# Kernel tuning notes

Hardware: AMD Instinct MI355X
Metric: run time of the kernel (lower is better)

## Reference

```python
import jax, jax.numpy as jnp
import numpy as np

EPS = 1e-5
NUM_GRAPHS = 64


def _linear(x, W, b):
    return x @ W + b


def setup_inputs() -> dict:
    key = jax.random.key(0)
    ks = jax.random.split(key, 32)
    N, E, IN, EF, H, ED, T, L, C = 25000, 400000, 128, 16, 32, 32, 4, 2, 1
    F = H            # F_in (divide_input=False)
    Fo = H // T      # F_out per tower

    def w(k, shape):
        return jax.random.normal(k, shape, jnp.float32) / np.sqrt(shape[-2])

    inp = {
        'x': jax.random.normal(ks[0], (N, IN), jnp.float32),
        'edge_attr': jax.random.normal(ks[1], (E, EF), jnp.float32),
        'edge_weight': jax.random.uniform(ks[2], (E,), jnp.float32),
        'edge_index': jax.random.randint(ks[3], (2, E), 0, N),
        'batch': jnp.sort(jax.random.randint(ks[4], (N,), 0, NUM_GRAPHS)),
        'node_W': w(ks[5], (IN, H)), 'node_b': jnp.zeros((H,), jnp.float32),
        'edge_W': w(ks[6], (EF, ED)), 'edge_b': jnp.zeros((ED,), jnp.float32),
        'enc_W': w(ks[7], (L, ED, F)), 'enc_b': jnp.zeros((L, F), jnp.float32),
        'pre_W': w(ks[8], (L, T, 3 * F, F)), 'pre_b': jnp.zeros((L, T, F), jnp.float32),
        'post_W': w(ks[9], (L, T, 13 * F, Fo)), 'post_b': jnp.zeros((L, T, Fo), jnp.float32),
        'lin_W': w(ks[10], (L, H, H)), 'lin_b': jnp.zeros((L, H), jnp.float32),
        'bn_g': jnp.ones((L, H), jnp.float32), 'bn_b': jnp.zeros((L, H), jnp.float32),
        'mlp_W1': w(ks[11], (H, H)), 'mlp_b1': jnp.zeros((H,), jnp.float32),
        'mlp_W2': w(ks[12], (H, H // 2)), 'mlp_b2': jnp.zeros((H // 2,), jnp.float32),
        'mlp_W3': w(ks[13], (H // 2, C)), 'mlp_b3': jnp.zeros((C,), jnp.float32),
    }
    return inp


def reference(x, edge_attr, edge_weight, node_W, node_b, edge_W, edge_b,
              enc_W, enc_b, pre_W, pre_b, post_W, post_b, lin_W, lin_b,
              bn_g, bn_b, mlp_W1, mlp_b1, mlp_W2, mlp_b2, mlp_W3, mlp_b3,
              edge_index, batch):
    N = x.shape[0]
    L, T = pre_W.shape[0], pre_W.shape[1]
    src, dst = edge_index[0], edge_index[1]

    # degree-based scalers (PNA): avg_deg_log = mean_n log(deg_n + 1)
    deg = jax.ops.segment_sum(jnp.ones((src.shape[0],), x.dtype), dst, num_segments=N)
    avg_deg_log = jnp.mean(jnp.log(deg + 1.0))
    degc = jnp.clip(deg, 1.0)[:, None, None]          # [N,1,1]
    log_deg = jnp.log(degc + 1.0)
    amp = log_deg / avg_deg_log                        # amplification scaler
    att = avg_deg_log / log_deg                        # attenuation scaler
    has_edge = (deg > 0)[:, None, None]

    h = _linear(x, node_W, node_b)                     # node_emb  [N,H]
    e = _linear(edge_attr, edge_W, edge_b)             # edge_emb  [E,ED]

    for l in range(L):
        el = _linear(e, enc_W[l], enc_b[l])            # edge_encoder [E,F]
        m_in = jnp.concatenate([h[dst], h[src], el], axis=-1)      # [E,3F]
        msg = jnp.einsum('ef,tfg->etg', m_in, pre_W[l]) + pre_b[l]  # per-tower pre_nn [E,T,F]
        msg = msg * edge_weight[:, None, None]
        s = jax.ops.segment_sum(msg, dst, num_segments=N)
        s2 = jax.ops.segment_sum(msg * msg, dst, num_segments=N)
        mean = s / degc
        std = jnp.sqrt(jax.nn.relu(s2 / degc - mean * mean) + EPS)
        mn = jnp.where(has_edge, jax.ops.segment_min(msg, dst, num_segments=N), 0.0)
        mx = jnp.where(has_edge, jax.ops.segment_max(msg, dst, num_segments=N), 0.0)
        agg = jnp.concatenate([mean, mn, mx, std], axis=-1)            # [N,T,4F]
        agg = jnp.concatenate([agg, agg * amp, agg * att], axis=-1)    # [N,T,12F]
        out = jnp.concatenate(
            [jnp.broadcast_to(h[:, None, :], (N, T, h.shape[-1])), agg], axis=-1)  # [N,T,13F]
        out = jnp.einsum('ntf,tfg->ntg', out, post_W[l]) + post_b[l]   # post_nn [N,T,Fo]
        out = out.reshape(N, -1) @ lin_W[l] + lin_b[l]                 # [N,H]
        mu = jnp.mean(out, axis=0)
        var = jnp.var(out, axis=0)
        out = (out - mu) / jnp.sqrt(var + EPS) * bn_g[l] + bn_b[l]     # BatchNorm (batch stats)
        h = jax.nn.relu(out)

    g = jax.ops.segment_sum(h, batch, num_segments=NUM_GRAPHS)        # global_add_pool
    g = jax.nn.relu(_linear(g, mlp_W1, mlp_b1))
    g = jax.nn.relu(_linear(g, mlp_W2, mlp_b2))
    return _linear(g, mlp_W3, mlp_b3)
```

## Files before the change

kernel.cpp:

```cpp
#include <hip/hip_runtime.h>

constexpr float kEps = 1e-5f;

typedef float f2v __attribute__((ext_vector_type(2)));

__device__ __forceinline__ unsigned short f2bf(float x) {
  unsigned int u = __float_as_uint(x);
  unsigned int r = (u + 0x7fffu + ((u >> 16) & 1u)) >> 16;
  return (unsigned short)r;
}
__device__ __forceinline__ float bflo(unsigned int u) { return __uint_as_float(u << 16); }
__device__ __forceinline__ float bfhi(unsigned int u) { return __uint_as_float(u & 0xffff0000u); }
__device__ __forceinline__ unsigned int packbf(float a, float b) {
  return (unsigned int)f2bf(a) | ((unsigned int)f2bf(b) << 16);
}
__device__ __forceinline__ f2v fma2(f2v a, f2v b, f2v c) { return __builtin_elementwise_fma(a, b, c); }
__device__ __forceinline__ f2v splat2(float x) { f2v r; r.x = x; r.y = x; return r; }
__device__ __forceinline__ f2v unpk(unsigned int u) { f2v r; r.x = bflo(u); r.y = bfhi(u); return r; }
__device__ __forceinline__ f2v min2(f2v a, f2v b) { return __builtin_elementwise_min(a, b); }
__device__ __forceinline__ f2v max2(f2v a, f2v b) { return __builtin_elementwise_max(a, b); }


__global__ void zero_kernel(int* __restrict__ a, int* __restrict__ b,
                            float* __restrict__ bnb, int n) {
  int i = blockIdx.x * blockDim.x + threadIdx.x;
  if (i < n) { a[i] = 0; b[i] = 0; }
  if (i < 128) bnb[i] = 0.f;
}

__global__ void hist_kernel(const int* __restrict__ dst, int* __restrict__ deg, int E) {
  int e = blockIdx.x * blockDim.x + threadIdx.x;
  if (e < E) atomicAdd(&deg[dst[e]], 1);
}

__global__ void scan1_kernel(const int* __restrict__ deg, int* __restrict__ off,
                             int* __restrict__ part, int N) {
  __shared__ int sm[1024];
  int i = blockIdx.x * 1024 + threadIdx.x;
  int v = (i < N) ? deg[i] : 0;
  sm[threadIdx.x] = v;
  __syncthreads();
  for (int o = 1; o < 1024; o <<= 1) {
    int t = (threadIdx.x >= o) ? sm[threadIdx.x - o] : 0;
    __syncthreads();
    sm[threadIdx.x] += t;
    __syncthreads();
  }
  if (i < N) off[i] = sm[threadIdx.x] - v;
  if (threadIdx.x == 1023) part[blockIdx.x] = sm[1023];
}

__global__ void scan2_kernel(int* __restrict__ part, int* __restrict__ off, int nb, int N) {
  if (threadIdx.x == 0) {
    int run = 0;
    for (int b = 0; b < nb; b++) { int p = part[b]; part[b] = run; run += p; }
    off[N] = run;
  }
}

__global__ void scan3_kernel(int* __restrict__ off, const int* __restrict__ part, int N) {
  int i = blockIdx.x * 1024 + threadIdx.x;
  if (i < N) off[i] += part[blockIdx.x];
}

__global__ void fill_kernel(const int* __restrict__ src, const int* __restrict__ dst,
                            const float* __restrict__ ew, const float4* __restrict__ eattr4,
                            const int* __restrict__ off, int* __restrict__ cnt,
                            int* __restrict__ srcs, float* __restrict__ ews,
                            float4* __restrict__ eattrg4, int E) {
  int e = blockIdx.x * blockDim.x + threadIdx.x;
  if (e < E) {
    int d = dst[e];
    int slot = off[d] + atomicAdd(&cnt[d], 1);
    srcs[slot] = src[e];
    ews[slot] = ew[e];
    float4 a = eattr4[e * 4 + 0], b = eattr4[e * 4 + 1];
    float4 c = eattr4[e * 4 + 2], q = eattr4[e * 4 + 3];
    eattrg4[(size_t)slot * 4 + 0] = a;
    eattrg4[(size_t)slot * 4 + 1] = b;
    eattrg4[(size_t)slot * 4 + 2] = c;
    eattrg4[(size_t)slot * 4 + 3] = q;
  }
}

__global__ void adl_kernel(const int* __restrict__ deg, float* __restrict__ adl, int N) {
  __shared__ float sm[1024];
  float s = 0.f;
  for (int n = threadIdx.x; n < N; n += 1024) s += logf((float)deg[n] + 1.f);
  sm[threadIdx.x] = s;
  __syncthreads();
  for (int o = 512; o > 0; o >>= 1) {
    if (threadIdx.x < o) sm[threadIdx.x] += sm[threadIdx.x + o];
    __syncthreads();
  }
  if (threadIdx.x == 0) adl[0] = sm[0];
}

__global__ void node_emb_kernel(const float* __restrict__ x, const float* __restrict__ W,
                                const float* __restrict__ b, float* __restrict__ h, int N) {
  int n = blockIdx.x * 8 + (threadIdx.x >> 5);
  int j = threadIdx.x & 31;
  if (n >= N) return;
  float acc = b[j];
  const float4* x4 = (const float4*)(x + (size_t)n * 128);
#pragma unroll
  for (int q = 0; q < 32; q++) {
    float4 v = x4[q];
    acc += v.x * W[(4 * q + 0) * 32 + j];
    acc += v.y * W[(4 * q + 1) * 32 + j];
    acc += v.z * W[(4 * q + 2) * 32 + j];
    acc += v.w * W[(4 * q + 3) * 32 + j];
  }
  h[n * 32 + j] = acc;
}

__global__ void fuse_kernel(const float* __restrict__ edge_W, const float* __restrict__ edge_b,
                            const float* __restrict__ enc_W, const float* __restrict__ enc_b,
                            const float* __restrict__ pre_W, const float* __restrict__ pre_b,
                            float* __restrict__ Wf, float* __restrict__ bf) {
  __shared__ float tW[2][16][32];
  __shared__ float tb[2][32];
  int tid = threadIdx.x;
  for (int i = tid; i < 1024; i += 256) {
    int l = i >> 9, r = (i >> 5) & 15, c = i & 31;
    float s = 0.f;
    for (int k = 0; k < 32; k++) s += edge_W[r * 32 + k] * enc_W[(l * 32 + k) * 32 + c];
    tW[l][r][c] = s;
  }
  for (int i = tid; i < 64; i += 256) {
    int l = i >> 5, c = i & 31;
    float s = enc_b[l * 32 + c];
    for (int k = 0; k < 32; k++) s += edge_b[k] * enc_W[(l * 32 + k) * 32 + c];
    tb[l][c] = s;
  }
  __syncthreads();
  for (int i = tid; i < 4096; i += 256) {
    int l = i >> 11, t = (i >> 9) & 3, r = (i >> 5) & 15, c = i & 31;
    float s = 0.f;
    for (int k = 0; k < 32; k++) s += tW[l][r][k] * pre_W[((l * 4 + t) * 96 + 64 + k) * 32 + c];
    Wf[i] = s;
  }
  for (int i = tid; i < 256; i += 256) {
    int l = i >> 7, t = (i >> 5) & 3, c = i & 31;
    float s = pre_b[(l * 4 + t) * 32 + c];
    for (int k = 0; k < 32; k++) s += tb[l][k] * pre_W[((l * 4 + t) * 96 + 64 + k) * 32 + c];
    bf[i] = s;
  }
}

__global__ __launch_bounds__(256) void prep_kernel(
    const float* __restrict__ h, const float* __restrict__ preW,
    const float* __restrict__ bfv, unsigned short* __restrict__ qB,
    unsigned short* __restrict__ AB, int N) {
  __shared__ float hs[16][32];
  int tid = threadIdx.x;
  int c = tid & 127, half = tid >> 7;
  int t = c >> 5, g = c & 31;
  float ws[32], wd[32];
  {
    const float* pS = preW + (t * 96 + 32) * 32 + g;
    const float* pD = preW + (t * 96) * 32 + g;
#pragma unroll
    for (int k = 0; k < 32; k++) { ws[k] = pS[k * 32]; wd[k] = pD[k * 32]; }
  }
  float bc = bfv[c];
  int base = blockIdx.x * 16;
  for (int i = tid; i < 512; i += 256) {
    int nn = i >> 5;
    hs[nn][i & 31] = (base + nn < N) ? h[(size_t)(base + nn) * 32 + (i & 31)] : 0.f;
  }
  __syncthreads();
#pragma unroll
  for (int nn = 0; nn < 8; ++nn) {
    int nl = half + 2 * nn;
    int n = base + nl;
    if (n >= N) continue;
    float qa = 0.f, Aa = bc;
#pragma unroll
    for (int k = 0; k < 32; k++) {
      float hk = hs[nl][k];
      qa = fmaf(hk, ws[k], qa);
      Aa = fmaf(hk, wd[k], Aa);
    }
    qB[(size_t)n * 128 + c] = f2bf(qa);
    AB[(size_t)n * 128 + c] = f2bf(Aa);
  }
}

__global__ __launch_bounds__(256) void bnprep_kernel(
    const float* __restrict__ pre, const float* __restrict__ bnv,
    const float* __restrict__ gamma, const float* __restrict__ beta,
    const float* __restrict__ preW, const float* __restrict__ bfv,
    float* __restrict__ h, unsigned short* __restrict__ qB,
    unsigned short* __restrict__ AB, int N) {
  __shared__ float hs[16][32];
  int tid = threadIdx.x;
  int base = blockIdx.x * 16;
  float invN = 1.f / (float)N;
  for (int idx = tid; idx < 512; idx += 256) {
    int nn = idx >> 5, j = idx & 31;
    int n = base + nn;
    float v = 0.f;
    if (n < N) {
      float mu = bnv[j] * invN;
      float var = bnv[32 + j] * invN - mu * mu;
      float is = rsqrtf(var + kEps);
      v = fmaxf((pre[(size_t)n * 32 + j] - mu) * is * gamma[j] + beta[j], 0.f);
      h[(size_t)n * 32 + j] = v;
    }
    hs[nn][j] = v;
  }
  int c = tid & 127, half = tid >> 7;
  int t = c >> 5, g = c & 31;
  float ws[32], wd[32];
  {
    const float* pS = preW + (t * 96 + 32) * 32 + g;
    const float* pD = preW + (t * 96) * 32 + g;
#pragma unroll
    for (int k = 0; k < 32; k++) { ws[k] = pS[k * 32]; wd[k] = pD[k * 32]; }
  }
  float bc = bfv[c];
  __syncthreads();
#pragma unroll
  for (int nn = 0; nn < 8; ++nn) {
    int nl = half + 2 * nn;
    int n = base + nl;
    if (n >= N) continue;
    float qa = 0.f, Aa = bc;
#pragma unroll
    for (int k = 0; k < 32; k++) {
      float hk = hs[nl][k];
      qa = fmaf(hk, ws[k], qa);
      Aa = fmaf(hk, wd[k], Aa);
    }
    qB[(size_t)n * 128 + c] = f2bf(qa);
    AB[(size_t)n * 128 + c] = f2bf(Aa);
  }
}

#define FOLDE(F, EA, EB, EC, ED)                                \
  F = fma2(splat2(EA.x), wf[0], F);  F = fma2(splat2(EA.y), wf[1], F);  \
  F = fma2(splat2(EA.z), wf[2], F);  F = fma2(splat2(EA.w), wf[3], F);  \
  F = fma2(splat2(EB.x), wf[4], F);  F = fma2(splat2(EB.y), wf[5], F);  \
  F = fma2(splat2(EB.z), wf[6], F);  F = fma2(splat2(EB.w), wf[7], F);  \
  F = fma2(splat2(EC.x), wf[8], F);  F = fma2(splat2(EC.y), wf[9], F);  \
  F = fma2(splat2(EC.z), wf[10], F); F = fma2(splat2(EC.w), wf[11], F); \
  F = fma2(splat2(ED.x), wf[12], F); F = fma2(splat2(ED.y), wf[13], F); \
  F = fma2(splat2(ED.z), wf[14], F); F = fma2(splat2(ED.w), wf[15], F);

#define STAT2(V)                                                \
  sum = sum + V; sq = fma2(V, V, sq); mn = min2(mn, V); mx = max2(mx, V);

__global__ __launch_bounds__(256, 3) void agg4_kernel(
    const unsigned int* __restrict__ qB, const unsigned int* __restrict__ AB,
    const int* __restrict__ coff, const int* __restrict__ srcs,
    const float* __restrict__ ews, const float* __restrict__ eattrg,
    const float* __restrict__ Wf, unsigned int* __restrict__ stats, int N) {
  int lane = threadIdx.x & 63;
  int n = (blockIdx.x * blockDim.x + threadIdx.x) >> 6;
  if (n >= N) return;
  int t = lane >> 4, g0 = (2 * lane) & 31;
  f2v wf[16];
  {
    const float* p = Wf + t * 512 + g0;
#pragma unroll
    for (int k = 0; k < 16; k++) { f2v r; r.x = p[k * 32]; r.y = p[k * 32 + 1]; wf[k] = r; }
  }
  f2v a = unpk(AB[(size_t)n * 64 + lane]);
  int beg = coff[n], end = coff[n + 1];
  int dg = end - beg;
  f2v sum = splat2(0.f), sq = splat2(0.f);
  f2v mn = splat2(1e30f), mx = splat2(-1e30f);

  int i = beg;
  int sc0 = 0, sc1 = 0, sc2 = 0, sc3 = 0;
  float w0 = 0.f, w1 = 0.f, w2 = 0.f, w3 = 0.f;
  if (i + 4 <= end) {
    sc0 = srcs[i]; sc1 = srcs[i + 1]; sc2 = srcs[i + 2]; sc3 = srcs[i + 3];
    w0 = ews[i]; w1 = ews[i + 1]; w2 = ews[i + 2]; w3 = ews[i + 3];
  }
  for (; i + 4 <= end; i += 4) {
    unsigned int q0 = qB[(size_t)sc0 * 64 + lane];
    unsigned int q1 = qB[(size_t)sc1 * 64 + lane];
    unsigned int q2 = qB[(size_t)sc2 * 64 + lane];
    unsigned int q3 = qB[(size_t)sc3 * 64 + lane];
    const float4* ep = (const float4*)(eattrg + (size_t)i * 16);
    float4 e0 = ep[0], e1 = ep[1], e2 = ep[2], e3 = ep[3];
    float4 e4 = ep[4], e5 = ep[5], e6 = ep[6], e7 = ep[7];
    float4 e8 = ep[8], e9 = ep[9], e10 = ep[10], e11 = ep[11];
    float4 e12 = ep[12], e13 = ep[13], e14 = ep[14], e15 = ep[15];
    float wc0 = w0, wc1 = w1, wc2 = w2, wc3 = w3;
    if (i + 8 <= end) {
      sc0 = srcs[i + 4]; sc1 = srcs[i + 5]; sc2 = srcs[i + 6]; sc3 = srcs[i + 7];
      w0 = ews[i + 4]; w1 = ews[i + 5]; w2 = ews[i + 6]; w3 = ews[i + 7];
    }
    __builtin_amdgcn_sched_barrier(0);
    f2v f0 = splat2(0.f), f1 = splat2(0.f), f2_ = splat2(0.f), f3 = splat2(0.f);
    FOLDE(f0, e0, e1, e2, e3)
    FOLDE(f1, e4, e5, e6, e7)
    FOLDE(f2_, e8, e9, e10, e11)
    FOLDE(f3, e12, e13, e14, e15)
    f2v v;
    v = (a + unpk(q0) + f0) * splat2(wc0); STAT2(v)
    v = (a + unpk(q1) + f1) * splat2(wc1); STAT2(v)
    v = (a + unpk(q2) + f2_) * splat2(wc2); STAT2(v)
    v = (a + unpk(q3) + f3) * splat2(wc3); STAT2(v)
  }
  for (; i < end; ++i) {
    int s = srcs[i];
    float w = ews[i];
    unsigned int q = qB[(size_t)s * 64 + lane];
    const float4* ep = (const float4*)(eattrg + (size_t)i * 16);
    float4 ea = ep[0], eb = ep[1], ec = ep[2], ed = ep[3];
    f2v f = splat2(0.f);
    FOLDE(f, ea, eb, ec, ed)
    f2v v = (a + unpk(q) + f) * splat2(w);
    STAT2(v)
  }
  if (dg == 0) { mn = splat2(0.f); mx = splat2(0.f); }
  float inv = 1.f / (float)(dg > 0 ? dg : 1);
  f2v mean = sum * splat2(inv);
  f2v var = sq * splat2(inv) - mean * mean;
  float sd0 = sqrtf(fmaxf(var.x, 0.f) + kEps);
  float sd1 = sqrtf(fmaxf(var.y, 0.f) + kEps);
  unsigned int* sp = stats + (size_t)n * 256;
  sp[0 * 64 + lane] = packbf(mean.x, mean.y);
  sp[1 * 64 + lane] = packbf(mn.x, mn.y);
  sp[2 * 64 + lane] = packbf(mx.x, mx.y);
  sp[3 * 64 + lane] = packbf(sd0, sd1);
}

__global__ __launch_bounds__(256) void post_kernel(
    const float* __restrict__ h, const unsigned int* __restrict__ stats,
    const int* __restrict__ coff, const float* __restrict__ adl,
    const float* __restrict__ postW, const float* __restrict__ postB,
    const float* __restrict__ linW, const float* __restrict__ linB,
    float* __restrict__ pre, float* __restrict__ bn, int N) {
  __shared__ unsigned int pwp[208 * 32];
  __shared__ unsigned int stu[4][256];
  __shared__ float red[8][32];
  int tid = threadIdx.x;
  for (int i = tid; i < 6656; i += 256) {
    int r = i >> 5, cc = i & 31, tP = cc >> 3, gq = cc & 7;
    float lo = postW[tP * 3328 + (2 * r) * 8 + gq];
    float hi = postW[tP * 3328 + (2 * r + 1) * 8 + gq];
    pwp[i] = packbf(lo, hi);
  }
  __syncthreads();

  int wave = tid >> 6, lane = tid & 63;
  int c = lane & 31, hh = lane >> 5;
  int tP = c >> 3;
  float adN = adl[0];
  float bs = 0.f, bq = 0.f;

  for (int n = blockIdx.x * 4 + wave; n < N; n += gridDim.x * 4) {
    {
      uint4 su = ((const uint4*)stats)[(size_t)n * 64 + lane];
      ((uint4*)stu[wave])[lane] = su;
    }
    int dg = coff[n + 1] - coff[n];
    float degc = (float)(dg > 0 ? dg : 1);
    float ad = adN / (float)N;
    float ld = logf(degc + 1.f);
    float amp = ld / ad, att = ad / ld;

    float acc = (hh == 0) ? postB[tP * 8 + (c & 7)] : 0.f;
    const float4* h4 = (const float4*)(h + (size_t)n * 32);
#pragma unroll
    for (int q4 = 0; q4 < 4; q4++) {
      float4 hv = h4[hh * 4 + q4];
      int r0 = hh * 8 + q4 * 2;
      unsigned int u0 = pwp[r0 * 32 + c], u1 = pwp[(r0 + 1) * 32 + c];
      acc = fmaf(hv.x, bflo(u0), acc);
      acc = fmaf(hv.y, bfhi(u0), acc);
      acc = fmaf(hv.z, bflo(u1), acc);
      acc = fmaf(hv.w, bfhi(u1), acc);
    }
#pragma unroll 8
    for (int jj = 0; jj < 32; jj++) {
      int sIdx = hh * 2 + (jj >> 4);
      unsigned int sv = stu[wave][sIdx * 64 + tP * 16 + (jj & 15)];
      float v0 = bflo(sv), v1 = bfhi(sv);
      int rm = 16 + hh * 32 + jj, ra = 80 + hh * 32 + jj, rt = 144 + hh * 32 + jj;
      unsigned int um = pwp[rm * 32 + c];
      unsigned int ua = pwp[ra * 32 + c];
      unsigned int ut = pwp[rt * 32 + c];
      float w0 = bflo(um); w0 = fmaf(amp, bflo(ua), w0); w0 = fmaf(att, bflo(ut), w0);
      float w1 = bfhi(um); w1 = fmaf(amp, bfhi(ua), w1); w1 = fmaf(att, bfhi(ut), w1);
      acc = fmaf(v0, w0, acc);
      acc = fmaf(v1, w1, acc);
    }
    acc += __shfl_xor(acc, 32);
    float o = linB[c];
#pragma unroll
    for (int k = 0; k < 32; k++) {
      float a = __shfl(acc, k);
      o = fmaf(a, linW[k * 32 + c], o);
    }
    if (lane < 32) {
      pre[(size_t)n * 32 + c] = o;
      bs += o;
      bq = fmaf(o, o, bq);
    }
  }

  __syncthreads();
  if (lane < 32) {
    red[wave * 2 + 0][c] = bs;
    red[wave * 2 + 1][c] = bq;
  }
  __syncthreads();
  if (tid < 64) {
    int which = tid >> 5, cc = tid & 31;
    float s = red[0 * 2 + which][cc] + red[1 * 2 + which][cc] +
              red[2 * 2 + which][cc] + red[3 * 2 + which][cc];
    atomicAdd(&bn[which * 32 + cc], s);
  }
}

__global__ void bn_apply_kernel(const float* __restrict__ pre, const float* __restrict__ bn,
                                const float* __restrict__ gamma, const float* __restrict__ beta,
                                float* __restrict__ h, int N) {
  int i = blockIdx.x * 256 + threadIdx.x;
  if (i >= N * 32) return;
  int j = i & 31;
  float invN = 1.f / (float)N;
  float mu = bn[j] * invN;
  float var = bn[32 + j] * invN - mu * mu;
  float is = rsqrtf(var + kEps);
  float v = (pre[i] - mu) * is * gamma[j] + beta[j];
  h[i] = fmaxf(v, 0.f);
}


__device__ __forceinline__ int lower_bound_dev(const int* a, int n, int key) {
  int lo = 0, hi = n;
  while (lo < hi) {
    int m = (lo + hi) >> 1;
    if (a[m] < key) lo = m + 1; else hi = m;
  }
  return lo;
}

__global__ void pool_kernel(const float* __restrict__ h, const int* __restrict__ batch,
                            float* __restrict__ gp, int N) {
  int gi = blockIdx.x;
  int lo = lower_bound_dev(batch, N, gi);
  int hi = lower_bound_dev(batch, N, gi + 1);
  __shared__ float part[8][32];
  int j = threadIdx.x & 31, ch = threadIdx.x >> 5;
  float s = 0.f;
  for (int n = lo + ch; n < hi; n += 8) s += h[(size_t)n * 32 + j];
  part[ch][j] = s;
  __syncthreads();
  if (threadIdx.x < 32) {
    float t = 0.f;
    for (int c2 = 0; c2 < 8; c2++) t += part[c2][j];
    gp[gi * 32 + j] = t;
  }
}

__global__ void mlp_kernel(const float* __restrict__ gp,
                           const float* __restrict__ W1, const float* __restrict__ b1,
                           const float* __restrict__ W2, const float* __restrict__ b2,
                           const float* __restrict__ W3, const float* __restrict__ b3,
                           float* __restrict__ out) {
  __shared__ float g1[64 * 32];
  __shared__ float g2[64 * 16];
  int tid = threadIdx.x;
  for (int i = tid; i < 2048; i += 256) {
    int r = i >> 5, c = i & 31;
    float s = b1[c];
    for (int k = 0; k < 32; k++) s += gp[r * 32 + k] * W1[k * 32 + c];
    g1[i] = fmaxf(s, 0.f);
  }
  __syncthreads();
  for (int i = tid; i < 1024; i += 256) {
    int r = i >> 4, c = i & 15;
    float s = b2[c];
    for (int k = 0; k < 32; k++) s += g1[r * 32 + k] * W2[k * 16 + c];
    g2[i] = fmaxf(s, 0.f);
  }
  __syncthreads();
  if (tid < 64) {
    float s = b3[0];
    for (int k = 0; k < 16; k++) s += g2[tid * 16 + k] * W3[k];
    out[tid] = s;
  }
}


extern "C" void kernel_launch(void* const* d_in, const int* in_sizes, int n_in,
                              void* d_out, int out_size, void* d_ws, size_t ws_size,
                              hipStream_t stream) {
  (void)n_in; (void)out_size; (void)ws_size;
  const float* x     = (const float*)d_in[0];
  const float* eattr = (const float*)d_in[1];
  const float* ew    = (const float*)d_in[2];
  const int*   eidx  = (const int*)d_in[3];
  const int*   batch = (const int*)d_in[4];
  const float* nodeW = (const float*)d_in[5];
  const float* nodeB = (const float*)d_in[6];
  const float* edgeW = (const float*)d_in[7];
  const float* edgeB = (const float*)d_in[8];
  const float* encW  = (const float*)d_in[9];
  const float* encB  = (const float*)d_in[10];
  const float* preW  = (const float*)d_in[11];
  const float* preB  = (const float*)d_in[12];
  const float* postW = (const float*)d_in[13];
  const float* postB = (const float*)d_in[14];
  const float* linW  = (const float*)d_in[15];
  const float* linB  = (const float*)d_in[16];
  const float* bnG   = (const float*)d_in[17];
  const float* bnB   = (const float*)d_in[18];
  const float* W1    = (const float*)d_in[19];
  const float* b1    = (const float*)d_in[20];
  const float* W2    = (const float*)d_in[21];
  const float* b2    = (const float*)d_in[22];
  const float* W3    = (const float*)d_in[23];
  const float* b3    = (const float*)d_in[24];
  float* out = (float*)d_out;

  int N = in_sizes[0] / 128;
  int E = in_sizes[2];
  const int* srcp = eidx;
  const int* dstp = eidx + E;

  char* wsb = (char*)d_ws;
  size_t woff = 0;
  auto alloc = [&](size_t bytes) -> void* {
    void* p = (void*)(wsb + woff);
    woff += (bytes + 255) & ~(size_t)255;
    return p;
  };
  int* deg   = (int*)alloc((size_t)N * 4);
  int* cnt   = (int*)alloc((size_t)N * 4);
  int* coff  = (int*)alloc((size_t)(N + 1) * 4);
  int* part  = (int*)alloc(64 * 4);
  int* srcs  = (int*)alloc((size_t)E * 4);
  float* ews = (float*)alloc((size_t)E * 4);
  float* eattrg = (float*)alloc((size_t)E * 16 * 4);
  float* h    = (float*)alloc((size_t)N * 32 * 4);
  float* pre  = (float*)alloc((size_t)N * 32 * 4);
  float* adl  = (float*)alloc(256);
  float* bnbuf = (float*)alloc(2 * 64 * 4);
  float* gp   = (float*)alloc(64 * 32 * 4);
  float* WfB  = (float*)alloc(2 * 4 * 16 * 32 * 4);
  float* bfB  = (float*)alloc(2 * 4 * 32 * 4);
  unsigned short* qB  = (unsigned short*)alloc((size_t)N * 128 * 2);
  unsigned short* AB  = (unsigned short*)alloc((size_t)N * 128 * 2);
  unsigned int* stats = (unsigned int*)alloc((size_t)N * 256 * 4);

  int nb = (N + 1023) / 1024;
  zero_kernel<<<(N + 255) / 256, 256, 0, stream>>>(deg, cnt, bnbuf, N);
  hist_kernel<<<(E + 255) / 256, 256, 0, stream>>>(dstp, deg, E);
  scan1_kernel<<<nb, 1024, 0, stream>>>(deg, coff, part, N);
  scan2_kernel<<<1, 64, 0, stream>>>(part, coff, nb, N);
  scan3_kernel<<<nb, 1024, 0, stream>>>(coff, part, N);
  fill_kernel<<<(E + 255) / 256, 256, 0, stream>>>(srcp, dstp, ew, (const float4*)eattr,
                                                   coff, cnt, srcs, ews, (float4*)eattrg, E);
  adl_kernel<<<1, 1024, 0, stream>>>(deg, adl, N);
  node_emb_kernel<<<(N + 7) / 8, 256, 0, stream>>>(x, nodeW, nodeB, h, N);
  fuse_kernel<<<1, 256, 0, stream>>>(edgeW, edgeB, encW, encB, preW, preB, WfB, bfB);

  prep_kernel<<<(N + 15) / 16, 256, 0, stream>>>(h, preW, bfB, qB, AB, N);
  agg4_kernel<<<(N + 3) / 4, 256, 0, stream>>>(
      (const unsigned int*)qB, (const unsigned int*)AB, coff, srcs, ews,
      eattrg, WfB, stats, N);
  post_kernel<<<1280, 256, 0, stream>>>(
      h, stats, coff, adl, postW, postB, linW, linB, pre, bnbuf, N);
  bnprep_kernel<<<(N + 15) / 16, 256, 0, stream>>>(
      pre, bnbuf, bnG, bnB, preW + 12288, bfB + 128, h, qB, AB, N);
  agg4_kernel<<<(N + 3) / 4, 256, 0, stream>>>(
      (const unsigned int*)qB, (const unsigned int*)AB, coff, srcs, ews,
      eattrg, WfB + 2048, stats, N);
  post_kernel<<<1280, 256, 0, stream>>>(
      h, stats, coff, adl, postW + 13312, postB + 32, linW + 1024, linB + 32,
      pre, bnbuf + 64, N);
  bn_apply_kernel<<<(N * 32 + 255) / 256, 256, 0, stream>>>(
      pre, bnbuf + 64, bnG + 32, bnB + 32, h, N);

  pool_kernel<<<64, 256, 0, stream>>>(h, batch, gp, N);
  mlp_kernel<<<1, 256, 0, stream>>>(gp, W1, b1, W2, b2, W3, b3, out);
}
```

Before: 454.2 us.

## Split edge-feature folding into separate kernel, store edge attrs as bf16, fuse BN into pool

Edge attributes are stored as bf16 in CSR order. A new efold kernel precomputes the per-edge 16->128 folded projection once per layer into a bf16 buffer. The aggregation kernel then only loads precomputed folded features, with 8-wide source unrolling and higher occupancy. When workspace is limited, the work is chunked over node ranges. The final BN-apply kernel is merged into the pooling kernel. This trades redundant per-lane FMA work and fp32 edge traffic for an extra write and read of a 256 B-per-edge intermediate, plus some bf16 precision loss.

```diff
diff --git a/kernel.cpp b/kernel.cpp
--- a/kernel.cpp
+++ b/kernel.cpp
@@ -67,7 +67,7 @@
                             const float* __restrict__ ew, const float4* __restrict__ eattr4,
                             const int* __restrict__ off, int* __restrict__ cnt,
                             int* __restrict__ srcs, float* __restrict__ ews,
-                            float4* __restrict__ eattrg4, int E) {
+                            uint4* __restrict__ egp, int E) {
   int e = blockIdx.x * blockDim.x + threadIdx.x;
   if (e < E) {
     int d = dst[e];
@@ -76,10 +76,13 @@
     ews[slot] = ew[e];
     float4 a = eattr4[e * 4 + 0], b = eattr4[e * 4 + 1];
     float4 c = eattr4[e * 4 + 2], q = eattr4[e * 4 + 3];
-    eattrg4[(size_t)slot * 4 + 0] = a;
-    eattrg4[(size_t)slot * 4 + 1] = b;
-    eattrg4[(size_t)slot * 4 + 2] = c;
-    eattrg4[(size_t)slot * 4 + 3] = q;
+    uint4 u0, u1;
+    u0.x = packbf(a.x, a.y); u0.y = packbf(a.z, a.w);
+    u0.z = packbf(b.x, b.y); u0.w = packbf(b.z, b.w);
+    u1.x = packbf(c.x, c.y); u1.y = packbf(c.z, c.w);
+    u1.z = packbf(q.x, q.y); u1.w = packbf(q.z, q.w);
+    egp[(size_t)slot * 2 + 0] = u0;
+    egp[(size_t)slot * 2 + 1] = u1;
   }
 }
 
@@ -238,27 +241,26 @@
   }
 }
 
-#define FOLDE(F, EA, EB, EC, ED)                                \
-  F = fma2(splat2(EA.x), wf[0], F);  F = fma2(splat2(EA.y), wf[1], F);  \
-  F = fma2(splat2(EA.z), wf[2], F);  F = fma2(splat2(EA.w), wf[3], F);  \
-  F = fma2(splat2(EB.x), wf[4], F);  F = fma2(splat2(EB.y), wf[5], F);  \
-  F = fma2(splat2(EB.z), wf[6], F);  F = fma2(splat2(EB.w), wf[7], F);  \
-  F = fma2(splat2(EC.x), wf[8], F);  F = fma2(splat2(EC.y), wf[9], F);  \
-  F = fma2(splat2(EC.z), wf[10], F); F = fma2(splat2(EC.w), wf[11], F); \
-  F = fma2(splat2(ED.x), wf[12], F); F = fma2(splat2(ED.y), wf[13], F); \
-  F = fma2(splat2(ED.z), wf[14], F); F = fma2(splat2(ED.w), wf[15], F);
-
-#define STAT2(V)                                                \
-  sum = sum + V; sq = fma2(V, V, sq); mn = min2(mn, V); mx = max2(mx, V);
-
-__global__ __launch_bounds__(256, 3) void agg4_kernel(
-    const unsigned int* __restrict__ qB, const unsigned int* __restrict__ AB,
-    const int* __restrict__ coff, const int* __restrict__ srcs,
-    const float* __restrict__ ews, const float* __restrict__ eattrg,
-    const float* __restrict__ Wf, unsigned int* __restrict__ stats, int N) {
+#define FOLDP(F, UA, UB)                                                       \
+  { f2v p;                                                                     \
+    p = unpk(UA.x); F = fma2(splat2(p.x), wf[0], F);  F = fma2(splat2(p.y), wf[1], F);  \
+    p = unpk(UA.y); F = fma2(splat2(p.x), wf[2], F);  F = fma2(splat2(p.y), wf[3], F);  \
+    p = unpk(UA.z); F = fma2(splat2(p.x), wf[4], F);  F = fma2(splat2(p.y), wf[5], F);  \
+    p = unpk(UA.w); F = fma2(splat2(p.x), wf[6], F);  F = fma2(splat2(p.y), wf[7], F);  \
+    p = unpk(UB.x); F = fma2(splat2(p.x), wf[8], F);  F = fma2(splat2(p.y), wf[9], F);  \
+    p = unpk(UB.y); F = fma2(splat2(p.x), wf[10], F); F = fma2(splat2(p.y), wf[11], F); \
+    p = unpk(UB.z); F = fma2(splat2(p.x), wf[12], F); F = fma2(splat2(p.y), wf[13], F); \
+    p = unpk(UB.w); F = fma2(splat2(p.x), wf[14], F); F = fma2(splat2(p.y), wf[15], F); }
+
+__global__ __launch_bounds__(256, 8) void efold_kernel(
+    const uint4* __restrict__ egp, const float* __restrict__ Wf,
+    unsigned int* __restrict__ eattrF, const int* __restrict__ coff,
+    int n0, int n1, int bound) {
   int lane = threadIdx.x & 63;
-  int n = (blockIdx.x * blockDim.x + threadIdx.x) >> 6;
-  if (n >= N) return;
+  int wv = (blockIdx.x * blockDim.x + threadIdx.x) >> 6;
+  int s0 = coff[n0], s1 = coff[n1];
+  int base = s0 + wv * 2;
+  if (base >= s1) return;
   int t = lane >> 4, g0 = (2 * lane) & 31;
   f2v wf[16];
   {
@@ -266,55 +268,87 @@
 #pragma unroll
     for (int k = 0; k < 16; k++) { f2v r; r.x = p[k * 32]; r.y = p[k * 32 + 1]; wf[k] = r; }
   }
+  uint4 ua = egp[(size_t)base * 2], ub = egp[(size_t)base * 2 + 1];
+  bool has1 = (base + 1 < s1);
+  uint4 uc, ud;
+  if (has1) { uc = egp[(size_t)(base + 1) * 2]; ud = egp[(size_t)(base + 1) * 2 + 1]; }
+  f2v f0 = splat2(0.f);
+  FOLDP(f0, ua, ub)
+  int idx0 = base - s0;
+  if (idx0 < bound) eattrF[(size_t)idx0 * 64 + lane] = packbf(f0.x, f0.y);
+  if (has1) {
+    f2v f1 = splat2(0.f);
+    FOLDP(f1, uc, ud)
+    int idx1 = idx0 + 1;
+    if (idx1 < bound) eattrF[(size_t)idx1 * 64 + lane] = packbf(f1.x, f1.y);
+  }
+}
+
+#define STAT2(V)                                                \
+  sum = sum + V; sq = fma2(V, V, sq); mn = min2(mn, V); mx = max2(mx, V);
+
+__global__ __launch_bounds__(256, 8) void agg5_kernel(
+    const unsigned int* __restrict__ qB, const unsigned int* __restrict__ AB,
+    const int* __restrict__ coff, const int* __restrict__ srcs,
+    const float* __restrict__ ews, const unsigned int* __restrict__ eattrF,
+    unsigned int* __restrict__ stats, int n0, int n1, int bound) {
+  int lane = threadIdx.x & 63;
+  int n = n0 + ((blockIdx.x * blockDim.x + threadIdx.x) >> 6);
+  if (n >= n1) return;
+  int s0c = coff[n0];
   f2v a = unpk(AB[(size_t)n * 64 + lane]);
   int beg = coff[n], end = coff[n + 1];
   int dg = end - beg;
   f2v sum = splat2(0.f), sq = splat2(0.f);
   f2v mn = splat2(1e30f), mx = splat2(-1e30f);
-
+  int bm = bound - 1;
   int i = beg;
-  int sc0 = 0, sc1 = 0, sc2 = 0, sc3 = 0;
-  float w0 = 0.f, w1 = 0.f, w2 = 0.f, w3 = 0.f;
-  if (i + 4 <= end) {
-    sc0 = srcs[i]; sc1 = srcs[i + 1]; sc2 = srcs[i + 2]; sc3 = srcs[i + 3];
-    w0 = ews[i]; w1 = ews[i + 1]; w2 = ews[i + 2]; w3 = ews[i + 3];
-  }
-  for (; i + 4 <= end; i += 4) {
-    unsigned int q0 = qB[(size_t)sc0 * 64 + lane];
-    unsigned int q1 = qB[(size_t)sc1 * 64 + lane];
-    unsigned int q2 = qB[(size_t)sc2 * 64 + lane];
-    unsigned int q3 = qB[(size_t)sc3 * 64 + lane];
-    const float4* ep = (const float4*)(eattrg + (size_t)i * 16);
-    float4 e0 = ep[0], e1 = ep[1], e2 = ep[2], e3 = ep[3];
-    float4 e4 = ep[4], e5 = ep[5], e6 = ep[6], e7 = ep[7];
-    float4 e8 = ep[8], e9 = ep[9], e10 = ep[10], e11 = ep[11];
-    float4 e12 = ep[12], e13 = ep[13], e14 = ep[14], e15 = ep[15];
-    float wc0 = w0, wc1 = w1, wc2 = w2, wc3 = w3;
+  int sA0 = 0, sA1 = 0, sA2 = 0, sA3 = 0, sA4 = 0, sA5 = 0, sA6 = 0, sA7 = 0;
+  if (i + 8 <= end) {
+    sA0 = srcs[i];     sA1 = srcs[i + 1]; sA2 = srcs[i + 2]; sA3 = srcs[i + 3];
+    sA4 = srcs[i + 4]; sA5 = srcs[i + 5]; sA6 = srcs[i + 6]; sA7 = srcs[i + 7];
+  }
+  for (; i + 8 <= end;) {
+    unsigned int q0 = qB[(size_t)sA0 * 64 + lane];
+    unsigned int q1 = qB[(size_t)sA1 * 64 + lane];
+    unsigned int q2 = qB[(size_t)sA2 * 64 + lane];
+    unsigned int q3 = qB[(size_t)sA3 * 64 + lane];
+    unsigned int q4 = qB[(size_t)sA4 * 64 + lane];
+    unsigned int q5 = qB[(size_t)sA5 * 64 + lane];
+    unsigned int q6 = qB[(size_t)sA6 * 64 + lane];
+    unsigned int q7 = qB[(size_t)sA7 * 64 + lane];
+    int ib = i - s0c;
+    unsigned int f0 = eattrF[(size_t)min(ib + 0, bm) * 64 + lane];
+    unsigned int f1 = eattrF[(size_t)min(ib + 1, bm) * 64 + lane];
+    unsigned int f2_ = eattrF[(size_t)min(ib + 2, bm) * 64 + lane];
+    unsigned int f3 = eattrF[(size_t)min(ib + 3, bm) * 64 + lane];
+    unsigned int f4 = eattrF[(size_t)min(ib + 4, bm) * 64 + lane];
+    unsigned int f5 = eattrF[(size_t)min(ib + 5, bm) * 64 + lane];
+    unsigned int f6 = eattrF[(size_t)min(ib + 6, bm) * 64 + lane];
+    unsigned int f7 = eattrF[(size_t)min(ib + 7, bm) * 64 + lane];
+    float w0 = ews[i],     w1 = ews[i + 1], w2 = ews[i + 2], w3 = ews[i + 3];
+    float w4 = ews[i + 4], w5 = ews[i + 5], w6 = ews[i + 6], w7 = ews[i + 7];
+    i += 8;
     if (i + 8 <= end) {
-      sc0 = srcs[i + 4]; sc1 = srcs[i + 5]; sc2 = srcs[i + 6]; sc3 = srcs[i + 7];
-      w0 = ews[i + 4]; w1 = ews[i + 5]; w2 = ews[i + 6]; w3 = ews[i + 7];
-    }
-    __builtin_amdgcn_sched_barrier(0);
-    f2v f0 = splat2(0.f), f1 = splat2(0.f), f2_ = splat2(0.f), f3 = splat2(0.f);
-    FOLDE(f0, e0, e1, e2, e3)
-    FOLDE(f1, e4, e5, e6, e7)
-    FOLDE(f2_, e8, e9, e10, e11)
-    FOLDE(f3, e12, e13, e14, e15)
+      sA0 = srcs[i];     sA1 = srcs[i + 1]; sA2 = srcs[i + 2]; sA3 = srcs[i + 3];
+      sA4 = srcs[i + 4]; sA5 = srcs[i + 5]; sA6 = srcs[i + 6]; sA7 = srcs[i + 7];
+    }
     f2v v;
-    v = (a + unpk(q0) + f0) * splat2(wc0); STAT2(v)
-    v = (a + unpk(q1) + f1) * splat2(wc1); STAT2(v)
-    v = (a + unpk(q2) + f2_) * splat2(wc2); STAT2(v)
-    v = (a + unpk(q3) + f3) * splat2(wc3); STAT2(v)
+    v = (a + unpk(q0) + unpk(f0)) * splat2(w0); STAT2(v)
+    v = (a + unpk(q1) + unpk(f1)) * splat2(w1); STAT2(v)
+    v = (a + unpk(q2) + unpk(f2_)) * splat2(w2); STAT2(v)
+    v = (a + unpk(q3) + unpk(f3)) * splat2(w3); STAT2(v)
+    v = (a + unpk(q4) + unpk(f4)) * splat2(w4); STAT2(v)
+    v = (a + unpk(q5) + unpk(f5)) * splat2(w5); STAT2(v)
+    v = (a + unpk(q6) + unpk(f6)) * splat2(w6); STAT2(v)
+    v = (a + unpk(q7) + unpk(f7)) * splat2(w7); STAT2(v)
   }
   for (; i < end; ++i) {
     int s = srcs[i];
+    unsigned int q = qB[(size_t)s * 64 + lane];
+    unsigned int f = eattrF[(size_t)min(i - s0c, bm) * 64 + lane];
     float w = ews[i];
-    unsigned int q = qB[(size_t)s * 64 + lane];
-    const float4* ep = (const float4*)(eattrg + (size_t)i * 16);
-    float4 ea = ep[0], eb = ep[1], ec = ep[2], ed = ep[3];
-    f2v f = splat2(0.f);
-    FOLDE(f, ea, eb, ec, ed)
-    f2v v = (a + unpk(q) + f) * splat2(w);
+    f2v v = (a + unpk(q) + unpk(f)) * splat2(w);
     STAT2(v)
   }
   if (dg == 0) { mn = splat2(0.f); mx = splat2(0.f); }
@@ -419,20 +453,6 @@
   }
 }
 
-__global__ void bn_apply_kernel(const float* __restrict__ pre, const float* __restrict__ bn,
-                                const float* __restrict__ gamma, const float* __restrict__ beta,
-                                float* __restrict__ h, int N) {
-  int i = blockIdx.x * 256 + threadIdx.x;
-  if (i >= N * 32) return;
-  int j = i & 31;
-  float invN = 1.f / (float)N;
-  float mu = bn[j] * invN;
-  float var = bn[32 + j] * invN - mu * mu;
-  float is = rsqrtf(var + kEps);
-  float v = (pre[i] - mu) * is * gamma[j] + beta[j];
-  h[i] = fmaxf(v, 0.f);
-}
-
 
 __device__ __forceinline__ int lower_bound_dev(const int* a, int n, int key) {
   int lo = 0, hi = n;
@@ -443,15 +463,22 @@
   return lo;
 }
 
-__global__ void pool_kernel(const float* __restrict__ h, const int* __restrict__ batch,
-                            float* __restrict__ gp, int N) {
+__global__ void pool2_kernel(const float* __restrict__ pre, const float* __restrict__ bnv,
+                             const float* __restrict__ gamma, const float* __restrict__ beta,
+                             const int* __restrict__ batch, float* __restrict__ gp, int N) {
   int gi = blockIdx.x;
   int lo = lower_bound_dev(batch, N, gi);
   int hi = lower_bound_dev(batch, N, gi + 1);
   __shared__ float part[8][32];
   int j = threadIdx.x & 31, ch = threadIdx.x >> 5;
+  float invN = 1.f / (float)N;
+  float mu = bnv[j] * invN;
+  float var = bnv[32 + j] * invN - mu * mu;
+  float is = rsqrtf(var + kEps);
+  float gm = gamma[j], bt = beta[j];
   float s = 0.f;
-  for (int n = lo + ch; n < hi; n += 8) s += h[(size_t)n * 32 + j];
+  for (int n = lo + ch; n < hi; n += 8)
+    s += fmaxf((pre[(size_t)n * 32 + j] - mu) * is * gm + bt, 0.f);
   part[ch][j] = s;
   __syncthreads();
   if (threadIdx.x < 32) {
@@ -494,7 +521,7 @@
 extern "C" void kernel_launch(void* const* d_in, const int* in_sizes, int n_in,
                               void* d_out, int out_size, void* d_ws, size_t ws_size,
                               hipStream_t stream) {
-  (void)n_in; (void)out_size; (void)ws_size;
+  (void)n_in; (void)out_size;
   const float* x     = (const float*)d_in[0];
   const float* eattr = (const float*)d_in[1];
   const float* ew    = (const float*)d_in[2];
@@ -540,7 +567,7 @@
   int* part  = (int*)alloc(64 * 4);
   int* srcs  = (int*)alloc((size_t)E * 4);
   float* ews = (float*)alloc((size_t)E * 4);
-  float* eattrg = (float*)alloc((size_t)E * 16 * 4);
+  unsigned int* egp = (unsigned int*)alloc((size_t)E * 32);
   float* h    = (float*)alloc((size_t)N * 32 * 4);
   float* pre  = (float*)alloc((size_t)N * 32 * 4);
   float* adl  = (float*)alloc(256);
@@ -552,6 +579,22 @@
   unsigned short* AB  = (unsigned short*)alloc((size_t)N * 128 * 2);
   unsigned int* stats = (unsigned int*)alloc((size_t)N * 256 * 4);
 
+  size_t fixed = woff;
+  size_t avail = (ws_size > fixed + (1u << 20)) ? (ws_size - fixed - (1u << 20)) : 0;
+  size_t cap_slots = avail / 256;
+  int k = 1;
+  if (cap_slots < (size_t)E) {
+    for (k = 2; k <= 64; ++k) {
+      size_t b = (size_t)E / k + (size_t)E / (k * 16) + 4096;
+      if (b <= cap_slots) break;
+    }
+  }
+  int bound = (k == 1) ? E : (int)((size_t)E / k + (size_t)E / (k * 16) + 4096);
+  unsigned int* eattrF = (unsigned int*)alloc((size_t)bound * 256);
+  int ncn = (N + k - 1) / k;
+  int grid_e = (bound + 7) / 8;
+  int grid_a = (ncn + 3) / 4;
+
   int nb = (N + 1023) / 1024;
   zero_kernel<<<(N + 255) / 256, 256, 0, stream>>>(deg, cnt, bnbuf, N);
   hist_kernel<<<(E + 255) / 256, 256, 0, stream>>>(dstp, deg, E);
@@ -559,28 +602,35 @@
   scan2_kernel<<<1, 64, 0, stream>>>(part, coff, nb, N);
   scan3_kernel<<<nb, 1024, 0, stream>>>(coff, part, N);
   fill_kernel<<<(E + 255) / 256, 256, 0, stream>>>(srcp, dstp, ew, (const float4*)eattr,
-                                                   coff, cnt, srcs, ews, (float4*)eattrg, E);
+                                                   coff, cnt, srcs, ews, (uint4*)egp, E);
   adl_kernel<<<1, 1024, 0, stream>>>(deg, adl, N);
   node_emb_kernel<<<(N + 7) / 8, 256, 0, stream>>>(x, nodeW, nodeB, h, N);
   fuse_kernel<<<1, 256, 0, stream>>>(edgeW, edgeB, encW, encB, preW, preB, WfB, bfB);
 
   prep_kernel<<<(N + 15) / 16, 256, 0, stream>>>(h, preW, bfB, qB, AB, N);
-  agg4_kernel<<<(N + 3) / 4, 256, 0, stream>>>(
-      (const unsigned int*)qB, (const unsigned int*)AB, coff, srcs, ews,
-      eattrg, WfB, stats, N);
+  for (int c = 0; c < k; ++c) {
+    int n0 = c * ncn, n1 = (n0 + ncn < N) ? n0 + ncn : N;
+    if (n0 >= n1) break;
+    efold_kernel<<<grid_e, 256, 0, stream>>>((const uint4*)egp, WfB, eattrF, coff, n0, n1, bound);
+    agg5_kernel<<<grid_a, 256, 0, stream>>>(
+        (const unsigned int*)qB, (const unsigned int*)AB, coff, srcs, ews,
+        eattrF, stats, n0, n1, bound);
+  }
   post_kernel<<<1280, 256, 0, stream>>>(
       h, stats, coff, adl, postW, postB, linW, linB, pre, bnbuf, N);
   bnprep_kernel<<<(N + 15) / 16, 256, 0, stream>>>(
       pre, bnbuf, bnG, bnB, preW + 12288, bfB + 128, h, qB, AB, N);
-  agg4_kernel<<<(N + 3) / 4, 256, 0, stream>>>(
-      (const unsigned int*)qB, (const unsigned int*)AB, coff, srcs, ews,
-      eattrg, WfB + 2048, stats, N);
+  for (int c = 0; c < k; ++c) {
+    int n0 = c * ncn, n1 = (n0 + ncn < N) ? n0 + ncn : N;
+    if (n0 >= n1) break;
+    efold_kernel<<<grid_e, 256, 0, stream>>>((const uint4*)egp, WfB + 2048, eattrF, coff, n0, n1, bound);
+    agg5_kernel<<<grid_a, 256, 0, stream>>>(
+        (const unsigned int*)qB, (const unsigned int*)AB, coff, srcs, ews,
+        eattrF, stats, n0, n1, bound);
+  }
   post_kernel<<<1280, 256, 0, stream>>>(
       h, stats, coff, adl, postW + 13312, postB + 32, linW + 1024, linB + 32,
       pre, bnbuf + 64, N);
-  bn_apply_kernel<<<(N * 32 + 255) / 256, 256, 0, stream>>>(
-      pre, bnbuf + 64, bnG + 32, bnB + 32, h, N);
-
-  pool_kernel<<<64, 256, 0, stream>>>(h, batch, gp, N);
+  pool2_kernel<<<64, 256, 0, stream>>>(pre, bnbuf + 64, bnG + 32, bnB + 32, batch, gp, N);
   mlp_kernel<<<1, 256, 0, stream>>>(gp, W1, b1, W2, b2, W3, b3, out);
 }
```

New measurement: 970.3 us. 114% more time.
